# Kernel tuning notes

Hardware: AMD Instinct MI355X
Metric: run time of the kernel (lower is better)

## Reference

```python
import jax, jax.numpy as jnp
import numpy as np

VEC = 90  # per-anchor vector length: obj(1)+box(4)+1 unused? -> layout: [p, dx, dy, dw, dh, _, 12 point, 72 seg]


def _decode(out, thresh, t, anchors, case):
    """Dense, mask-based version of Detector._filter + Detector._parse.

    The torch code gathers rows via nonzero (data-dependent shape); for a
    jit-compatible reference we decode every cell and zero out rows whose
    sigmoid(objectness) <= thresh. Row layout matches torch exactly:
    [n, sigmoid(p), cx, cy, w, h, point(12), seg(72)].
    """
    B, C, H, W = out.shape
    v = jnp.transpose(out, (0, 2, 3, 1)).reshape(B, H, W, 3, VEC)
    p = v[..., 0]
    mask = jax.nn.sigmoid(p) > thresh                      # [B,H,W,3]
    iy = jnp.arange(H, dtype=v.dtype)[None, :, None, None]
    ix = jnp.arange(W, dtype=v.dtype)[None, None, :, None]
    cy = (iy + v[..., 2]) * t
    cx = (ix + v[..., 1]) * t
    w = anchors[:, 0] * jnp.exp(v[..., 3])                 # broadcast over anchor dim
    h = anchors[:, 1] * jnp.exp(v[..., 4])
    s = jnp.sqrt(w * w + h * h) / case                     # diagonal / case, [B,H,W,3]
    point = v[..., 6:18] * s[..., None]                    # 6 (x,y) keypoint pairs scaled
    seg = v[..., 18:90].reshape(B, H, W, 3, 24, 3)         # 24 triplets (coord, sig, sig)
    seg = jnp.concatenate(
        [seg[..., :1] * s[..., None, None], jax.nn.sigmoid(seg[..., 1:3])],
        axis=-1).reshape(B, H, W, 3, 72)
    n = jnp.broadcast_to(jnp.arange(B, dtype=v.dtype)[:, None, None, None], p.shape)
    obj = jnp.stack([n, jax.nn.sigmoid(p), cx, cy, w, h], axis=-1)
    rows = jnp.concatenate([obj, point, seg], axis=-1).reshape(-1, VEC)
    return jnp.where(mask.reshape(-1, 1), rows, jnp.zeros((), rows.dtype))


def setup_inputs() -> dict:
    key = jax.random.key(0)
    ks = jax.random.split(key, 7)
    B = 32
    return {
        "out13": jax.random.normal(ks[0], (B, 270, 13, 13), jnp.float32),
        "out26": jax.random.normal(ks[1], (B, 270, 26, 26), jnp.float32),
        "out52": jax.random.normal(ks[2], (B, 270, 52, 52), jnp.float32),
        "anchors13": jax.random.uniform(ks[3], (3, 2), jnp.float32, 50.0, 300.0),
        "anchors26": jax.random.uniform(ks[4], (3, 2), jnp.float32, 20.0, 120.0),
        "anchors52": jax.random.uniform(ks[5], (3, 2), jnp.float32, 5.0, 60.0),
        "thresh": jax.random.uniform(ks[6], (1,), jnp.float32, 0.4, 0.7),
        "case": 416,
    }


def reference(out13, out26, out52, anchors13, anchors26, anchors52, thresh, case):
    th = thresh[0]
    c = jnp.float32(case)
    boxes = jnp.concatenate([
        _decode(out13, th, jnp.float32(32.0), anchors13, c),
        _decode(out26, th, jnp.float32(16.0), anchors26, c),
        _decode(out52, th, jnp.float32(8.0), anchors52, c),
    ], axis=0)
    return boxes
```

## Files before the change

### kernel.cpp

```cpp
#include <hip/hip_runtime.h>
#include <math.h>

#define NT  192
#define PXW 64
#define PXS 32
#define FR  48

typedef float vf4 __attribute__((ext_vector_type(4)));
typedef float vf2 __attribute__((ext_vector_type(2)));

__device__ __forceinline__ float sigf(float x) { return 1.0f / (1.0f + expf(-x)); }

__device__ __forceinline__ void ntflush4(const float* __restrict__ lds,
                                         float* __restrict__ outp, int nfl, int tid)
{
    vf4* d4 = (vf4*)outp;
    const vf4* s4 = (const vf4*)lds;
    for (int i = tid; i < (nfl >> 2); i += NT)
        __builtin_nontemporal_store(s4[i], d4 + i);
}
__device__ __forceinline__ void ntflush2(const float* __restrict__ lds,
                                         float* __restrict__ outp, int nfl, int tid)
{
    vf2* d2 = (vf2*)outp;
    const vf2* s2 = (const vf2*)lds;
    for (int i = tid; i < (nfl >> 1); i += NT)
        __builtin_nontemporal_store(s2[i], d2 + i);
}

template<int H, int W, int T>
__device__ __forceinline__ void decode_wide(
    const float* __restrict__ in, const float* __restrict__ anchors,
    float th, float invCase, float* __restrict__ out, long gRowBase,
    int blkL, float* __restrict__ lds)
{
    constexpr int HW = H * W;
    constexpr int SPANS = (HW + PXW - 1) / PXW;
    const int b    = blkL / SPANS;
    const int P0   = (blkL % SPANS) * PXW;
    const int npix = (HW - P0 < PXW) ? (HW - P0) : PXW;

    const int tid = threadIdx.x;
    const int a = tid >> 6, lane = tid & 63, h = lane >> 5, p2 = lane & 31;
    const int q0 = 2 * p2;
    const bool act = q0 < npix;

    float v0[45], v1[45];
    if (act) {
        const float* src = in + ((long)b * 270 + a * 90 + 45 * h) * HW + P0 + q0;
        #pragma unroll
        for (int j = 0; j < 45; ++j) {
            vf2 t2 = *(const vf2*)(src + (long)j * HW);
            v0[j] = t2.x; v1[j] = t2.y;
        }

        float sp0 = sigf(v0[0]), sp1 = sigf(v1[0]);
        bool  m0 = sp0 > th,     m1 = sp1 > th;
        float A0 = anchors[a * 2 + 0], A1 = anchors[a * 2 + 1];
        float w0 = A0 * expf(v0[3]), w1 = A0 * expf(v1[3]);
        float h0 = A1 * expf(v0[4]), h1 = A1 * expf(v1[4]);
        float s0 = sqrtf(w0 * w0 + h0 * h0) * invCase;
        float s1 = sqrtf(w1 * w1 + h1 * h1) * invCase;
        int pix0 = P0 + q0;
        int x0 = pix0 % W, y0 = pix0 / W;
        int x1 = (pix0 + 1) % W, y1 = (pix0 + 1) / W;
        float cx0 = ((float)x0 + v0[1]) * (float)T, cy0 = ((float)y0 + v0[2]) * (float)T;
        float cx1 = ((float)x1 + v1[1]) * (float)T, cy1 = ((float)y1 + v1[2]) * (float)T;

        float ms0 = __shfl(m0 ? s0 : 0.0f, p2, 64);
        float ms1 = __shfl(m1 ? s1 : 0.0f, p2, 64);
        float mf0 = __shfl(m0 ? 1.0f : 0.0f, p2, 64);
        float mf1 = __shfl(m1 ? 1.0f : 0.0f, p2, 64);
        const bool mB0 = mf0 > 0.5f, mB1 = mf1 > 0.5f;

        #pragma unroll
        for (int j = 0; j < 45; ++j) {
            bool coord = (j % 3 == 0), pt = (j >= 6 && j < 18);
            float a0 = v0[j], a1 = v1[j];
            if (coord)   { v0[j] = a0 * ms0;  v1[j] = a1 * ms1; }
            else if (pt) { v0[j] = (h == 0) ? a0 * ms0 : (mB0 ? sigf(a0) : 0.0f);
                           v1[j] = (h == 0) ? a1 * ms1 : (mB1 ? sigf(a1) : 0.0f); }
            else         { v0[j] = mB0 ? sigf(a0) : 0.0f;
                           v1[j] = mB1 ? sigf(a1) : 0.0f; }
        }
        if (h == 0) {
            v0[0] = m0 ? (float)b : 0.0f;  v1[0] = m1 ? (float)b : 0.0f;
            v0[1] = m0 ? sp0 : 0.0f;       v1[1] = m1 ? sp1 : 0.0f;
            v0[2] = m0 ? cx0 : 0.0f;       v1[2] = m1 ? cx1 : 0.0f;
            v0[3] = m0 ? cy0 : 0.0f;       v1[3] = m1 ? cy1 : 0.0f;
            v0[4] = m0 ? w0  : 0.0f;       v1[4] = m1 ? w1  : 0.0f;
            v0[5] = m0 ? h0  : 0.0f;       v1[5] = m1 ? h1  : 0.0f;
        }
    }

    const size_t gbase = (size_t)(gRowBase + ((long)b * HW + P0) * 3) * 90;
    const int myf = p2 >> 3;

    #pragma unroll
    for (int f = 0; f < PXW / 16; ++f) {
        int pf = npix - 16 * f;
        if (pf <= 0) break;
        if (pf > 16) pf = 16;
        if (act && myf == f) {
            float* dst = lds + ((q0 - 16 * f) * 3 + a) * 90 + 45 * h;
            #pragma unroll
            for (int j = 0; j < 45; ++j) dst[j] = v0[j];
            dst += 270;
            #pragma unroll
            for (int j = 0; j < 45; ++j) dst[j] = v1[j];
        }
        __syncthreads();
        ntflush4(lds, out + gbase + (size_t)f * FR * 90, pf * 3 * 90, tid);
        __syncthreads();
    }
}

__device__ __forceinline__ void decode13(
    const float* __restrict__ in, const float* __restrict__ anchors,
    float th, float invCase, float* __restrict__ out,
    int blkL, float* __restrict__ lds)
{
    constexpr int H = 13, W = 13, T = 32, HW = 169;
    constexpr int SPANS = (HW + PXS - 1) / PXS;
    const int b    = blkL / SPANS;
    const int P0   = (blkL % SPANS) * PXS;
    const int npix = (HW - P0 < PXS) ? (HW - P0) : PXS;

    const int tid = threadIdx.x;
    const int a = tid >> 6, lane = tid & 63, h = lane >> 5, p = lane & 31;
    const bool act = p < npix;

    float v[45];
    if (act) {
        const int pix = P0 + p;
        const int x = pix % W, y = pix / W;
        const float* src = in + ((long)b * 270 + a * 90 + 45 * h) * HW + pix;
        #pragma unroll
        for (int j = 0; j < 45; ++j) v[j] = src[(long)j * HW];

        float sp = sigf(v[0]);
        bool  m  = sp > th;
        float A0 = anchors[a * 2 + 0], A1 = anchors[a * 2 + 1];
        float w  = A0 * expf(v[3]);
        float hb = A1 * expf(v[4]);
        float s  = sqrtf(w * w + hb * hb) * invCase;
        float cx = ((float)x + v[1]) * (float)T;
        float cy = ((float)y + v[2]) * (float)T;

        float ms = __shfl(m ? s : 0.0f, p, 64);
        float mf = __shfl(m ? 1.0f : 0.0f, p, 64);
        const bool mB = mf > 0.5f;

        #pragma unroll
        for (int j = 0; j < 45; ++j) {
            float val = v[j];
            bool coord = (j % 3 == 0), pt = (j >= 6 && j < 18);
            if (coord)   v[j] = val * ms;
            else if (pt) v[j] = (h == 0) ? val * ms : (mB ? sigf(val) : 0.0f);
            else         v[j] = mB ? sigf(val) : 0.0f;
        }
        if (h == 0) {
            v[0] = m ? (float)b : 0.0f;
            v[1] = m ? sp       : 0.0f;
            v[2] = m ? cx       : 0.0f;
            v[3] = m ? cy       : 0.0f;
            v[4] = m ? w        : 0.0f;
            v[5] = m ? hb       : 0.0f;
        }
    }

    const size_t gbase = (size_t)(((long)b * HW + P0) * 3) * 90;

    if (act && p < 16) {
        float* dst = lds + (p * 3 + a) * 90 + 45 * h;
        #pragma unroll
        for (int j = 0; j < 45; ++j) dst[j] = v[j];
    }
    __syncthreads();
    int nA = npix < 16 ? npix : 16;
    ntflush2(lds, out + gbase, nA * 3 * 90, tid);

    int nB = npix - 16;
    if (nB > 0) {
        __syncthreads();
        if (act && p >= 16) {
            float* dst = lds + ((p - 16) * 3 + a) * 90 + 45 * h;
            #pragma unroll
            for (int j = 0; j < 45; ++j) dst[j] = v[j];
        }
        __syncthreads();
        ntflush2(lds, out + gbase + (size_t)FR * 90, nB * 3 * 90, tid);
    }
}

__global__ __launch_bounds__(NT, 4) void decode_all(
    const float* __restrict__ in13, const float* __restrict__ in26,
    const float* __restrict__ in52,
    const float* __restrict__ anc13, const float* __restrict__ anc26,
    const float* __restrict__ anc52,
    const float* __restrict__ thresh, const int* __restrict__ casep,
    float* __restrict__ out, int nblk52, int nblk26, long rows13, long rows26)
{
    __shared__ float lds[FR * 90];
    const float th = thresh[0];
    const float invCase = 1.0f / (float)(*casep);
    const int blk = blockIdx.x;

    if (blk < nblk52)
        decode_wide<52, 52, 8>(in52, anc52, th, invCase, out,
                               rows13 + rows26, blk, lds);
    else if (blk < nblk52 + nblk26)
        decode_wide<26, 26, 16>(in26, anc26, th, invCase, out,
                                rows13, blk - nblk52, lds);
    else
        decode13(in13, anc13, th, invCase, out, blk - nblk52 - nblk26, lds);
}

extern "C" void kernel_launch(void* const* d_in, const int* in_sizes, int n_in,
                              void* d_out, int out_size, void* d_ws, size_t ws_size,
                              hipStream_t stream) {
    const float* in13  = (const float*)d_in[0];
    const float* in26  = (const float*)d_in[1];
    const float* in52  = (const float*)d_in[2];
    const float* anc13 = (const float*)d_in[3];
    const float* anc26 = (const float*)d_in[4];
    const float* anc52 = (const float*)d_in[5];
    const float* th    = (const float*)d_in[6];
    const int*   casep = (const int*)d_in[7];
    float* out = (float*)d_out;

    int B = in_sizes[0] / (270 * 13 * 13);

    long rows13 = (long)B * 13 * 13 * 3;
    long rows26 = (long)B * 26 * 26 * 3;

    int nblk13 = B * ((13 * 13 + PXS - 1) / PXS);
    int nblk26 = B * ((26 * 26 + PXW - 1) / PXW);
    int nblk52 = B * ((52 * 52 + PXW - 1) / PXW);

    decode_all<<<dim3(nblk52 + nblk26 + nblk13), dim3(NT), 0, stream>>>(
        in13, in26, in52, anc13, anc26, anc52, th, casep, out,
        nblk52, nblk26, rows13, rows26);
}
```

Baseline: 54.92 us.

## Process two tiles per block with prefetch and use regular stores

Each wide-scale block now decodes two pixel spans, half a grid apart, in a loop. It prefetches the first five channels of the second span while the first span is being flushed, which halves the block count for the 26 and 52 scales. The output stores also switch from nontemporal to normal vector stores. The aim is to overlap load latency with the flush phase and cut block launch overhead, at the cost of fewer blocks in flight and possibly more cache pollution from the regular stores.

```diff
diff --git a/kernel.cpp b/kernel.cpp
--- a/kernel.cpp
+++ b/kernel.cpp
@@ -11,47 +11,63 @@
 
 __device__ __forceinline__ float sigf(float x) { return 1.0f / (1.0f + expf(-x)); }
 
-__device__ __forceinline__ void ntflush4(const float* __restrict__ lds,
-                                         float* __restrict__ outp, int nfl, int tid)
+__device__ __forceinline__ void flush4(const float* __restrict__ lds,
+                                       float* __restrict__ outp, int nfl, int tid)
 {
     vf4* d4 = (vf4*)outp;
     const vf4* s4 = (const vf4*)lds;
-    for (int i = tid; i < (nfl >> 2); i += NT)
-        __builtin_nontemporal_store(s4[i], d4 + i);
-}
-__device__ __forceinline__ void ntflush2(const float* __restrict__ lds,
-                                         float* __restrict__ outp, int nfl, int tid)
+    for (int i = tid; i < (nfl >> 2); i += NT) d4[i] = s4[i];
+}
+__device__ __forceinline__ void flush2(const float* __restrict__ lds,
+                                       float* __restrict__ outp, int nfl, int tid)
 {
     vf2* d2 = (vf2*)outp;
     const vf2* s2 = (const vf2*)lds;
-    for (int i = tid; i < (nfl >> 1); i += NT)
-        __builtin_nontemporal_store(s2[i], d2 + i);
+    for (int i = tid; i < (nfl >> 1); i += NT) d2[i] = s2[i];
 }
 
 template<int H, int W, int T>
 __device__ __forceinline__ void decode_wide(
     const float* __restrict__ in, const float* __restrict__ anchors,
     float th, float invCase, float* __restrict__ out, long gRowBase,
-    int blkL, float* __restrict__ lds)
+    int blk0, int halfSpan, float* __restrict__ lds)
 {
     constexpr int HW = H * W;
     constexpr int SPANS = (HW + PXW - 1) / PXW;
-    const int b    = blkL / SPANS;
-    const int P0   = (blkL % SPANS) * PXW;
-    const int npix = (HW - P0 < PXW) ? (HW - P0) : PXW;
-
     const int tid = threadIdx.x;
     const int a = tid >> 6, lane = tid & 63, h = lane >> 5, p2 = lane & 31;
     const int q0 = 2 * p2;
-    const bool act = q0 < npix;
-
-    float v0[45], v1[45];
-    if (act) {
+
+    float n0[5] = {0, 0, 0, 0, 0}, n1[5] = {0, 0, 0, 0, 0};
+    {
+        const int b = blk0 / SPANS, P0 = (blk0 % SPANS) * PXW;
+        const int npix = (HW - P0 < PXW) ? (HW - P0) : PXW;
+        if (q0 < npix) {
+            const float* src = in + ((long)b * 270 + a * 90 + 45 * h) * HW + P0 + q0;
+            #pragma unroll
+            for (int j = 0; j < 5; ++j) {
+                vf2 t2 = *(const vf2*)(src + (long)j * HW);
+                n0[j] = t2.x; n1[j] = t2.y;
+            }
+        }
+    }
+
+    for (int it = 0; it < 2; ++it) {
+        const int blkL = blk0 + it * halfSpan;
+        const int b = blkL / SPANS, P0 = (blkL % SPANS) * PXW;
+        const int npix = (HW - P0 < PXW) ? (HW - P0) : PXW;
+        const bool act = q0 < npix;
         const float* src = in + ((long)b * 270 + a * 90 + 45 * h) * HW + P0 + q0;
-        #pragma unroll
-        for (int j = 0; j < 45; ++j) {
-            vf2 t2 = *(const vf2*)(src + (long)j * HW);
-            v0[j] = t2.x; v1[j] = t2.y;
+
+        float v0[45], v1[45];
+        #pragma unroll
+        for (int j = 0; j < 5; ++j) { v0[j] = n0[j]; v1[j] = n1[j]; }
+        if (act) {
+            #pragma unroll
+            for (int j = 5; j < 45; ++j) {
+                vf2 t2 = *(const vf2*)(src + (long)j * HW);
+                v0[j] = t2.x; v1[j] = t2.y;
+            }
         }
 
         float sp0 = sigf(v0[0]), sp1 = sigf(v1[0]);
@@ -91,27 +107,41 @@
             v0[4] = m0 ? w0  : 0.0f;       v1[4] = m1 ? w1  : 0.0f;
             v0[5] = m0 ? h0  : 0.0f;       v1[5] = m1 ? h1  : 0.0f;
         }
-    }
-
-    const size_t gbase = (size_t)(gRowBase + ((long)b * HW + P0) * 3) * 90;
-    const int myf = p2 >> 3;
-
-    #pragma unroll
-    for (int f = 0; f < PXW / 16; ++f) {
-        int pf = npix - 16 * f;
-        if (pf <= 0) break;
-        if (pf > 16) pf = 16;
-        if (act && myf == f) {
-            float* dst = lds + ((q0 - 16 * f) * 3 + a) * 90 + 45 * h;
-            #pragma unroll
-            for (int j = 0; j < 45; ++j) dst[j] = v0[j];
-            dst += 270;
-            #pragma unroll
-            for (int j = 0; j < 45; ++j) dst[j] = v1[j];
-        }
-        __syncthreads();
-        ntflush4(lds, out + gbase + (size_t)f * FR * 90, pf * 3 * 90, tid);
-        __syncthreads();
+
+        if (it == 0) {
+            const int blkN = blk0 + halfSpan;
+            const int bN = blkN / SPANS, P0N = (blkN % SPANS) * PXW;
+            const int npixN = (HW - P0N < PXW) ? (HW - P0N) : PXW;
+            if (q0 < npixN) {
+                const float* srcN = in + ((long)bN * 270 + a * 90 + 45 * h) * HW + P0N + q0;
+                #pragma unroll
+                for (int j = 0; j < 5; ++j) {
+                    vf2 t2 = *(const vf2*)(srcN + (long)j * HW);
+                    n0[j] = t2.x; n1[j] = t2.y;
+                }
+            }
+        }
+
+        const size_t gbase = (size_t)(gRowBase + ((long)b * HW + P0) * 3) * 90;
+        const int myf = p2 >> 3;
+
+        #pragma unroll
+        for (int f = 0; f < PXW / 16; ++f) {
+            int pf = npix - 16 * f;
+            if (pf <= 0) break;
+            if (pf > 16) pf = 16;
+            if (act && myf == f) {
+                float* dst = lds + ((q0 - 16 * f) * 3 + a) * 90 + 45 * h;
+                #pragma unroll
+                for (int j = 0; j < 45; ++j) dst[j] = v0[j];
+                dst += 270;
+                #pragma unroll
+                for (int j = 0; j < 45; ++j) dst[j] = v1[j];
+            }
+            __syncthreads();
+            flush4(lds, out + gbase + (size_t)f * FR * 90, pf * 3 * 90, tid);
+            __syncthreads();
+        }
     }
 }
 
@@ -178,7 +208,7 @@
     }
     __syncthreads();
     int nA = npix < 16 ? npix : 16;
-    ntflush2(lds, out + gbase, nA * 3 * 90, tid);
+    flush2(lds, out + gbase, nA * 3 * 90, tid);
 
     int nB = npix - 16;
     if (nB > 0) {
@@ -189,7 +219,7 @@
             for (int j = 0; j < 45; ++j) dst[j] = v[j];
         }
         __syncthreads();
-        ntflush2(lds, out + gbase + (size_t)FR * 90, nB * 3 * 90, tid);
+        flush2(lds, out + gbase + (size_t)FR * 90, nB * 3 * 90, tid);
     }
 }
 
@@ -199,21 +229,21 @@
     const float* __restrict__ anc13, const float* __restrict__ anc26,
     const float* __restrict__ anc52,
     const float* __restrict__ thresh, const int* __restrict__ casep,
-    float* __restrict__ out, int nblk52, int nblk26, long rows13, long rows26)
+    float* __restrict__ out, int nb52h, int nb26h, long rows13, long rows26)
 {
     __shared__ float lds[FR * 90];
     const float th = thresh[0];
     const float invCase = 1.0f / (float)(*casep);
     const int blk = blockIdx.x;
 
-    if (blk < nblk52)
+    if (blk < nb52h)
         decode_wide<52, 52, 8>(in52, anc52, th, invCase, out,
-                               rows13 + rows26, blk, lds);
-    else if (blk < nblk52 + nblk26)
+                               rows13 + rows26, blk, nb52h, lds);
+    else if (blk < nb52h + nb26h)
         decode_wide<26, 26, 16>(in26, anc26, th, invCase, out,
-                                rows13, blk - nblk52, lds);
+                                rows13, blk - nb52h, nb26h, lds);
     else
-        decode13(in13, anc13, th, invCase, out, blk - nblk52 - nblk26, lds);
+        decode13(in13, anc13, th, invCase, out, blk - nb52h - nb26h, lds);
 }
 
 extern "C" void kernel_launch(void* const* d_in, const int* in_sizes, int n_in,
@@ -235,10 +265,10 @@
     long rows26 = (long)B * 26 * 26 * 3;
 
     int nblk13 = B * ((13 * 13 + PXS - 1) / PXS);
-    int nblk26 = B * ((26 * 26 + PXW - 1) / PXW);
-    int nblk52 = B * ((52 * 52 + PXW - 1) / PXW);
-
-    decode_all<<<dim3(nblk52 + nblk26 + nblk13), dim3(NT), 0, stream>>>(
+    int nb26h  = B * ((26 * 26 + PXW - 1) / PXW) / 2;
+    int nb52h  = B * ((52 * 52 + PXW - 1) / PXW) / 2;
+
+    decode_all<<<dim3(nb52h + nb26h + nblk13), dim3(NT), 0, stream>>>(
         in13, in26, in52, anc13, anc26, anc52, th, casep, out,
-        nblk52, nblk26, rows13, rows26);
-}
+        nb52h, nb26h, rows13, rows26);
+}
```

After: 67.65 us. 23.2% more time.
